# Kernel optimization log

Measured on AMD Instinct MI355X. Metric: run time of the kernel, lower is better.

## Reference

```python
import jax, jax.numpy as jnp
import numpy as np

EMB = 16
N_LEFT = 100000
N_RIGHT = 100000
N_EDGES = 3200000


def setup_inputs() -> dict:
    key = jax.random.key(0)
    ks = jax.random.split(key, 16)
    s = 1.0 / np.sqrt(EMB)
    inp = {
        "left_features": jax.random.normal(ks[0], (N_LEFT, EMB), jnp.float32),
        "edge_indices": jax.random.randint(ks[1], (2, N_EDGES), 0, N_RIGHT, jnp.int64) if jax.config.jax_enable_x64 else jax.random.randint(ks[1], (2, N_EDGES), 0, N_RIGHT, jnp.int32),
        "edge_features": jax.random.normal(ks[2], (N_EDGES, 1), jnp.float32),
        "right_features": jax.random.normal(ks[3], (N_RIGHT, EMB), jnp.float32),
        # feature_module_left: Linear(emb, emb, bias=True)
        "W_left": jax.random.uniform(ks[4], (EMB, EMB), jnp.float32, -s, s),
        "b_left": jax.random.uniform(ks[5], (EMB,), jnp.float32, -s, s),
        # feature_module_edge: Linear(1, emb, bias=False)
        "W_edge": jax.random.uniform(ks[6], (1, EMB), jnp.float32, -1.0, 1.0),
        # feature_module_right: Linear(emb, emb, bias=False)
        "W_right": jax.random.uniform(ks[7], (EMB, EMB), jnp.float32, -s, s),
        # feature_module_final: ReLU -> Linear(emb, emb)
        "W_final": jax.random.uniform(ks[8], (EMB, EMB), jnp.float32, -s, s),
        "b_final": jax.random.uniform(ks[9], (EMB,), jnp.float32, -s, s),
        # post_conv_module: ReLU -> Linear(emb, emb)
        "W_post": jax.random.uniform(ks[10], (EMB, EMB), jnp.float32, -s, s),
        "b_post": jax.random.uniform(ks[11], (EMB,), jnp.float32, -s, s),
        # output_module: Linear(2*emb, emb) -> ReLU -> Linear(emb, emb)
        "W_out1": jax.random.uniform(ks[12], (2 * EMB, EMB), jnp.float32, -1.0 / np.sqrt(2 * EMB), 1.0 / np.sqrt(2 * EMB)),
        "b_out1": jax.random.uniform(ks[13], (EMB,), jnp.float32, -s, s),
        "W_out2": jax.random.uniform(ks[14], (EMB, EMB), jnp.float32, -s, s),
        "b_out2": jax.random.uniform(ks[15], (EMB,), jnp.float32, -s, s),
    }
    return inp


def reference(left_features, edge_indices, edge_features, right_features,
              W_left, b_left, W_edge, W_right, W_final, b_final,
              W_post, b_post, W_out1, b_out1, W_out2, b_out2):
    left_idx = edge_indices[0]
    right_idx = edge_indices[1]
    n_right = right_features.shape[0]

    # per-edge messages: [E, emb]
    msg_left = left_features[left_idx] @ W_left + b_left
    msg_edge = edge_features @ W_edge
    msg_right = right_features[right_idx] @ W_right
    messages = jax.nn.relu(msg_left + msg_edge + msg_right) @ W_final + b_final

    # scatter-add over right nodes
    aggregated = jax.ops.segment_sum(messages, right_idx, num_segments=n_right)

    post = jax.nn.relu(aggregated) @ W_post + b_post
    h = jnp.concatenate([post, right_features], axis=-1)  # [N_right, 2*emb]
    out = jax.nn.relu(h @ W_out1 + b_out1) @ W_out2 + b_out2
    return out
```

## Files before the change

### kernel.cpp

```cpp
#include <hip/hip_runtime.h>

#define EMB 16
#define NPB 196
#define BNODES 256
#define MAXNB 512
#define PCHUNK 6656
#define RPTC 13
#define MAXCHUNKS 512
#define REC_CAP 2048
#define RPT 4
typedef unsigned int u32;
typedef unsigned long long u64;

__global__ void zero_f32(float* __restrict__ p, size_t n) {
    size_t i = (size_t)blockIdx.x * blockDim.x + threadIdx.x;
    size_t stride = (size_t)gridDim.x * blockDim.x;
    for (; i < n; i += stride) p[i] = 0.0f;
}

__global__ void zero_i32(int* __restrict__ p, int n) {
    int i = blockIdx.x * blockDim.x + threadIdx.x;
    if (i < n) p[i] = 0;
}

__device__ __forceinline__ u32 bf16bits_rne(float x) {
    u32 u = __float_as_uint(x);
    return (u + 0x7fffu + ((u >> 16) & 1u)) >> 16;
}

__global__ void linear16_pack_kernel(const float* __restrict__ X, const float* __restrict__ W,
                                     const float* __restrict__ b, u32* __restrict__ Y, int N) {
    int tid = blockIdx.x * blockDim.x + threadIdx.x;
    int row = tid >> 3;
    int h = tid & 7;
    if (row >= N) return;
    float a0 = b ? b[h] : 0.0f;
    float a1 = b ? b[h + 8] : 0.0f;
    const float* xr = X + (size_t)row * EMB;
#pragma unroll
    for (int k = 0; k < EMB; ++k) {
        float xv = xr[k];
        a0 = fmaf(xv, W[k * EMB + h], a0);
        a1 = fmaf(xv, W[k * EMB + h + 8], a1);
    }
    Y[(size_t)row * 8 + h] = (bf16bits_rne(a1) << 16) | bf16bits_rne(a0);
}

__global__ void linear16_kernel(const float* __restrict__ X, const float* __restrict__ W,
                                const float* __restrict__ b, float* __restrict__ Y, int N) {
    int tid = blockIdx.x * blockDim.x + threadIdx.x;
    int row = tid >> 4;
    int j = tid & 15;
    if (row >= N) return;
    float acc = b ? b[j] : 0.0f;
    const float* xr = X + (size_t)row * EMB;
#pragma unroll
    for (int k = 0; k < EMB; ++k) acc = fmaf(xr[k], W[k * EMB + j], acc);
    Y[(size_t)row * EMB + j] = acc;
}

__launch_bounds__(512)
__global__ void chunk_sort_kernel(const int* __restrict__ eidx, const float* __restrict__ ef,
                                  u64* __restrict__ rec, int2* __restrict__ cbM,
                                  int E, int NB, int nchunks) {
    __shared__ u64 srec[PCHUNK];
    __shared__ int hist[MAXNB];
    __shared__ int wsum[8];
    int t = threadIdx.x;
    int lane = t & 63, wid = t >> 6;
    int c = blockIdx.x;
    long long base = (long long)c * PCHUNK;
    int n = (int)(((long long)E - base) < PCHUNK ? ((long long)E - base) : PCHUNK);
    const int* ridx = eidx + E;

    for (int i = t; i < NB; i += 512) hist[i] = 0;
    __syncthreads();
    u64 rcv[RPTC];
    int pk[RPTC];
#pragma unroll
    for (int k = 0; k < RPTC; ++k) {
        int i = t + k * 512;
        rcv[k] = 0; pk[k] = 0;
        if (i < n) {
            int r = ridx[base + i];
            int l = eidx[base + i];
            float f = ef[base + i];
            int bb = r / NPB;
            int rl = r - bb * NPB;
            int rank = atomicAdd(&hist[bb], 1);
            rcv[k] = ((u64)__float_as_uint(f) << 32) | ((u64)(u32)l << 8) | (u32)rl;
            pk[k] = (bb << 13) | rank;
        }
    }
    __syncthreads();
    int v = (t < NB) ? hist[t] : 0;
    int inc = v;
#pragma unroll
    for (int d = 1; d < 64; d <<= 1) {
        int x = __shfl_up(inc, d, 64);
        if (lane >= d) inc += x;
    }
    if (lane == 63) wsum[wid] = inc;
    __syncthreads();
    int off = 0;
#pragma unroll
    for (int w = 0; w < 8; ++w) off += (w < wid) ? wsum[w] : 0;
    int ex = off + inc - v;
    if (t < NB) {
        cbM[(size_t)t * nchunks + c] = make_int2(v, ex);
        hist[t] = ex;
    }
    __syncthreads();
#pragma unroll
    for (int k = 0; k < RPTC; ++k) {
        int i = t + k * 512;
        if (i < n) srec[hist[pk[k] >> 13] + (pk[k] & 8191)] = rcv[k];
    }
    __syncthreads();
    for (int i = t; i < n; i += 512) rec[base + i] = srec[i];
}

__launch_bounds__(512)
__global__ void bucket_gather_kernel(const u64* __restrict__ rec, const int2* __restrict__ cbM,
                                     const u32* __restrict__ Lpk, const u32* __restrict__ Rpk,
                                     const float* __restrict__ We, const float* __restrict__ rf,
                                     const float* __restrict__ Wf, const float* __restrict__ bf,
                                     const float* __restrict__ Wp, const float* __restrict__ bp,
                                     const float* __restrict__ Wo1, const float* __restrict__ bo1,
                                     const float* __restrict__ Wo2, const float* __restrict__ bo2,
                                     float* __restrict__ out,
                                     int n_right, int NB, int nchunks) {
    __shared__ u64 srec[REC_CAP];
    __shared__ u32 addrtab[REC_CAP];
    __shared__ int runsum[MAXCHUNKS + 1];
    __shared__ int rbase[MAXCHUNKS];
    __shared__ int hist[BNODES], base_[BNODES];
    __shared__ int wsum[8];
    __shared__ float sWf[256], sWp[256], sWo1[512], sWo2[256], sb[64];
    int b = blockIdx.x;
    int t = threadIdx.x;
    int lane = t & 63, wid = t >> 6;
    int node0 = b * NPB;

    if (t < 256) { sWf[t] = Wf[t]; sWp[t] = Wp[t]; sWo2[t] = Wo2[t]; }
    sWo1[t] = Wo1[t];
    if (t < 16) { sb[t] = bf[t]; sb[16 + t] = bp[t]; sb[32 + t] = bo1[t]; sb[48 + t] = bo2[t]; }

    int len = 0, cb = 0;
    if (t < nchunks) { int2 v = cbM[(size_t)b * nchunks + t]; len = v.x; cb = v.y; }
    int inc = len;
#pragma unroll
    for (int d = 1; d < 64; d <<= 1) {
        int x = __shfl_up(inc, d, 64);
        if (lane >= d) inc += x;
    }
    if (lane == 63) wsum[wid] = inc;
    __syncthreads();
    int off = 0;
#pragma unroll
    for (int w = 0; w < 8; ++w) off += (w < wid) ? wsum[w] : 0;
    int pexcl = off + inc - len;
    if (t < nchunks) { runsum[t] = pexcl; rbase[t] = t * PCHUNK + cb; }
    if (t == 511) runsum[nchunks] = off + inc;
    __syncthreads();
    int total = runsum[nchunks];

    int n = t >> 1, q = t & 1;
    int node = node0 + n;
    bool nv = (n < NPB) && (node < n_right);

    float we[16];
#pragma unroll
    for (int j = 0; j < 16; ++j) we[j] = We[j];

    float rv[16];
    if (nv) {
        const uint4* rp = (const uint4*)(Rpk + (size_t)node * 8);
        uint4 ra = rp[0], rb = rp[1];
        u32 w0 = ra.x, w1 = ra.y, w2 = ra.z, w3 = ra.w;
        u32 w4 = rb.x, w5 = rb.y, w6 = rb.z, w7 = rb.w;
        rv[0] = __uint_as_float(w0 << 16); rv[8]  = __uint_as_float(w0 & 0xffff0000u);
        rv[1] = __uint_as_float(w1 << 16); rv[9]  = __uint_as_float(w1 & 0xffff0000u);
        rv[2] = __uint_as_float(w2 << 16); rv[10] = __uint_as_float(w2 & 0xffff0000u);
        rv[3] = __uint_as_float(w3 << 16); rv[11] = __uint_as_float(w3 & 0xffff0000u);
        rv[4] = __uint_as_float(w4 << 16); rv[12] = __uint_as_float(w4 & 0xffff0000u);
        rv[5] = __uint_as_float(w5 << 16); rv[13] = __uint_as_float(w5 & 0xffff0000u);
        rv[6] = __uint_as_float(w6 << 16); rv[14] = __uint_as_float(w6 & 0xffff0000u);
        rv[7] = __uint_as_float(w7 << 16); rv[15] = __uint_as_float(w7 & 0xffff0000u);
    } else {
#pragma unroll
        for (int j = 0; j < 16; ++j) rv[j] = 0.0f;
    }

    float acc[16];
#pragma unroll
    for (int j = 0; j < 16; ++j) acc[j] = 0.0f;
    int dsum = 0;

    for (int tile0 = 0; tile0 < total; tile0 += REC_CAP) {
        int m = total - tile0; if (m > REC_CAP) m = REC_CAP;
        u64 rcl[RPT];
        int rnk[RPT];
        if (t < BNODES) hist[t] = 0;
        for (int r = t; r < nchunks; r += 512) {
            int g_lo = runsum[r], g_hi = runsum[r + 1];
            int lo = g_lo > tile0 ? g_lo : tile0;
            int hi = g_hi < tile0 + m ? g_hi : tile0 + m;
            int a = rbase[r] + (lo - g_lo);
            for (int g = lo; g < hi; ++g, ++a) addrtab[g - tile0] = (u32)a;
        }
        __syncthreads();
#pragma unroll
        for (int k = 0; k < RPT; ++k) {
            int i = t + k * 512;
            rcl[k] = (i < m) ? rec[(size_t)addrtab[i]] : 0;
        }
#pragma unroll
        for (int k = 0; k < RPT; ++k) {
            int i = t + k * 512;
            rnk[k] = (i < m) ? atomicAdd(&hist[(int)(rcl[k] & 0xffu)], 1) : 0;
        }
        __syncthreads();
        if (t < 64) {
            int h0 = hist[4 * t], h1 = hist[4 * t + 1], h2 = hist[4 * t + 2], h3 = hist[4 * t + 3];
            int s4 = h0 + h1 + h2 + h3;
            int inc4 = s4;
#pragma unroll
            for (int d = 1; d < 64; d <<= 1) {
                int x = __shfl_up(inc4, d, 64);
                if (t >= d) inc4 += x;
            }
            int ex = inc4 - s4;
            base_[4 * t] = ex;
            base_[4 * t + 1] = ex + h0;
            base_[4 * t + 2] = ex + h0 + h1;
            base_[4 * t + 3] = ex + h0 + h1 + h2;
        }
        __syncthreads();
#pragma unroll
        for (int k = 0; k < RPT; ++k) {
            int i = t + k * 512;
            if (i < m) srec[base_[(int)(rcl[k] & 0xffu)] + rnk[k]] = rcl[k];
        }
        __syncthreads();
        {
            int cc = nv ? hist[n] : 0;
            int b0_ = nv ? base_[n] : 0;
            if (q == 0) dsum += cc;
            for (int k = q; k < cc; k += 2) {
                u64 rc = srec[b0_ + k];
                int l = (int)((rc >> 8) & 0xFFFFFFu);
                float f = __uint_as_float((u32)(rc >> 32));
                const uint4* lp = (const uint4*)(Lpk + (size_t)l * 8);
                uint4 la = lp[0], lb = lp[1];
                u32 w0 = la.x, w1 = la.y, w2 = la.z, w3 = la.w;
                u32 w4 = lb.x, w5 = lb.y, w6 = lb.z, w7 = lb.w;
#define PAIR(h, lw) { \
                float l0 = __uint_as_float(lw << 16); \
                float l1 = __uint_as_float(lw & 0xffff0000u); \
                acc[h]     += fmaxf(fmaf(f, we[h], l0) + rv[h], 0.0f); \
                acc[h + 8] += fmaxf(fmaf(f, we[h + 8], l1) + rv[h + 8], 0.0f); }
                PAIR(0, w0) PAIR(1, w1) PAIR(2, w2) PAIR(3, w3)
                PAIR(4, w4) PAIR(5, w5) PAIR(6, w6) PAIR(7, w7)
#undef PAIR
            }
        }
        __syncthreads();
    }

#pragma unroll
    for (int j = 0; j < 16; ++j) acc[j] += __shfl_xor(acc[j], 1, 64);
    dsum += __shfl_xor(dsum, 1, 64);

    if (nv) {
        float rfx[16];
        const float4* Rf = (const float4*)(rf + (size_t)node * EMB);
#pragma unroll
        for (int k = 0; k < 4; ++k) {
            float4 w = Rf[k];
            rfx[4 * k] = w.x; rfx[4 * k + 1] = w.y; rfx[4 * k + 2] = w.z; rfx[4 * k + 3] = w.w;
        }
        float c = (float)dsum;
        float x[16], y[16], z[16], o[16];
#pragma unroll
        for (int j = 0; j < 16; ++j) {
            float a = c * sb[j];
#pragma unroll
            for (int k = 0; k < 16; ++k) a = fmaf(acc[k], sWf[k * 16 + j], a);
            x[j] = fmaxf(a, 0.0f);
        }
#pragma unroll
        for (int j = 0; j < 16; ++j) {
            float a = sb[16 + j];
#pragma unroll
            for (int k = 0; k < 16; ++k) a = fmaf(x[k], sWp[k * 16 + j], a);
            y[j] = a;
        }
#pragma unroll
        for (int j = 0; j < 16; ++j) {
            float a = sb[32 + j];
#pragma unroll
            for (int k = 0; k < 16; ++k) a = fmaf(y[k], sWo1[k * 16 + j], a);
#pragma unroll
            for (int k = 0; k < 16; ++k) a = fmaf(rfx[k], sWo1[(16 + k) * 16 + j], a);
            z[j] = fmaxf(a, 0.0f);
        }
#pragma unroll
        for (int j = 0; j < 16; ++j) {
            float a = sb[48 + j];
#pragma unroll
            for (int k = 0; k < 16; ++k) a = fmaf(z[k], sWo2[k * 16 + j], a);
            o[j] = a;
        }
        float4* Op = (float4*)(out + (size_t)node * EMB);
        Op[q * 2]     = make_float4(o[q * 8],     o[q * 8 + 1], o[q * 8 + 2], o[q * 8 + 3]);
        Op[q * 2 + 1] = make_float4(o[q * 8 + 4], o[q * 8 + 5], o[q * 8 + 6], o[q * 8 + 7]);
    }
}

__global__ void edge_kernel(const int* __restrict__ eidx, const float* __restrict__ ef,
                            const float* __restrict__ L, const float* __restrict__ R,
                            const float* __restrict__ We, float* __restrict__ S,
                            int* __restrict__ cnt, int E) {
    long long tid = (long long)blockIdx.x * blockDim.x + threadIdx.x;
    int e = (int)(tid >> 4);
    int j = (int)(tid & 15);
    if (e >= E) return;
    int l = eidx[e];
    int r = eidx[E + e];
    float v = L[(size_t)l * EMB + j] + ef[e] * We[j] + R[(size_t)r * EMB + j];
    v = fmaxf(v, 0.0f);
    unsafeAtomicAdd(&S[(size_t)r * EMB + j], v);
    if (j == 0) atomicAdd(&cnt[r], 1);
}

__global__ void final_kernel(const float* __restrict__ S, const int* __restrict__ deg,
                             const float* __restrict__ rf,
                             const float* __restrict__ Wf, const float* __restrict__ bf,
                             const float* __restrict__ Wp, const float* __restrict__ bp,
                             const float* __restrict__ Wo1, const float* __restrict__ bo1,
                             const float* __restrict__ Wo2, const float* __restrict__ bo2,
                             float* __restrict__ out, int N) {
    __shared__ float sWf[256], sWp[256], sWo1[512], sWo2[256];
    __shared__ float sb[64];
    int t = threadIdx.x;
    for (int i = t; i < 256; i += 256) { sWf[i] = Wf[i]; sWp[i] = Wp[i]; sWo2[i] = Wo2[i]; }
    for (int i = t; i < 512; i += 256) sWo1[i] = Wo1[i];
    if (t < 16) { sb[t] = bf[t]; sb[16 + t] = bp[t]; sb[32 + t] = bo1[t]; sb[48 + t] = bo2[t]; }
    __syncthreads();

    int r = blockIdx.x * blockDim.x + t;
    if (r >= N) return;

    float s[16], x[16], y[16], rv[16], z[16], o[16];
    const float4* Sp = (const float4*)(S + (size_t)r * EMB);
    const float4* Rp = (const float4*)(rf + (size_t)r * EMB);
#pragma unroll
    for (int k = 0; k < 4; ++k) {
        float4 v = Sp[k];
        s[4 * k] = v.x; s[4 * k + 1] = v.y; s[4 * k + 2] = v.z; s[4 * k + 3] = v.w;
        float4 w = Rp[k];
        rv[4 * k] = w.x; rv[4 * k + 1] = w.y; rv[4 * k + 2] = w.z; rv[4 * k + 3] = w.w;
    }
    float c = (float)deg[r];

#pragma unroll
    for (int j = 0; j < 16; ++j) {
        float a = c * sb[j];
#pragma unroll
        for (int k = 0; k < 16; ++k) a = fmaf(s[k], sWf[k * 16 + j], a);
        x[j] = fmaxf(a, 0.0f);
    }
#pragma unroll
    for (int j = 0; j < 16; ++j) {
        float a = sb[16 + j];
#pragma unroll
        for (int k = 0; k < 16; ++k) a = fmaf(x[k], sWp[k * 16 + j], a);
        y[j] = a;
    }
#pragma unroll
    for (int j = 0; j < 16; ++j) {
        float a = sb[32 + j];
#pragma unroll
        for (int k = 0; k < 16; ++k) a = fmaf(y[k], sWo1[k * 16 + j], a);
#pragma unroll
        for (int k = 0; k < 16; ++k) a = fmaf(rv[k], sWo1[(16 + k) * 16 + j], a);
        z[j] = fmaxf(a, 0.0f);
    }
#pragma unroll
    for (int j = 0; j < 16; ++j) {
        float a = sb[48 + j];
#pragma unroll
        for (int k = 0; k < 16; ++k) a = fmaf(z[k], sWo2[k * 16 + j], a);
        o[j] = a;
    }
    float4* Op = (float4*)(out + (size_t)r * EMB);
#pragma unroll
    for (int k = 0; k < 4; ++k)
        Op[k] = make_float4(o[4 * k], o[4 * k + 1], o[4 * k + 2], o[4 * k + 3]);
}

extern "C" void kernel_launch(void* const* d_in, const int* in_sizes, int n_in,
                              void* d_out, int out_size, void* d_ws, size_t ws_size,
                              hipStream_t stream) {
    const float* lf     = (const float*)d_in[0];
    const int*   eidx   = (const int*)d_in[1];
    const float* ef     = (const float*)d_in[2];
    const float* rf     = (const float*)d_in[3];
    const float* W_left = (const float*)d_in[4];
    const float* b_left = (const float*)d_in[5];
    const float* W_edge = (const float*)d_in[6];
    const float* W_right= (const float*)d_in[7];
    const float* W_final= (const float*)d_in[8];
    const float* b_final= (const float*)d_in[9];
    const float* W_post = (const float*)d_in[10];
    const float* b_post = (const float*)d_in[11];
    const float* W_out1 = (const float*)d_in[12];
    const float* b_out1 = (const float*)d_in[13];
    const float* W_out2 = (const float*)d_in[14];
    const float* b_out2 = (const float*)d_in[15];

    int n_left  = in_sizes[0] / EMB;
    int E       = in_sizes[2];
    int n_right = in_sizes[3] / EMB;
    float* out = (float*)d_out;

    int NB = (n_right + NPB - 1) / NPB;
    int nchunks = (E + PCHUNK - 1) / PCHUNK;

    size_t need = (size_t)E * 8
                + (size_t)NB * nchunks * 8
                + ((size_t)n_left + n_right) * 32;

    if (ws_size >= need && NB <= MAXNB && nchunks <= MAXCHUNKS) {
        u64*  rec = (u64*)d_ws;
        int2* cbM = (int2*)(rec + (size_t)E);
        u32*  Lpk = (u32*)(cbM + (size_t)NB * nchunks);
        u32*  Rpk = Lpk + (size_t)n_left * 8;

        linear16_pack_kernel<<<(n_left * 8 + 255) / 256, 256, 0, stream>>>(lf, W_left, b_left, Lpk, n_left);
        linear16_pack_kernel<<<(n_right * 8 + 255) / 256, 256, 0, stream>>>(rf, W_right, nullptr, Rpk, n_right);

        chunk_sort_kernel<<<nchunks, 512, 0, stream>>>(eidx, ef, rec, cbM, E, NB, nchunks);

        bucket_gather_kernel<<<NB, 512, 0, stream>>>(rec, cbM, Lpk, Rpk, W_edge, rf,
                                                     W_final, b_final, W_post, b_post,
                                                     W_out1, b_out1, W_out2, b_out2,
                                                     out, n_right, NB, nchunks);
    } else {
        float* L   = (float*)d_ws;
        float* R   = L + (size_t)n_left * EMB;
        float* S   = R + (size_t)n_right * EMB;
        int*   cnt = (int*)(S + (size_t)n_right * EMB);

        zero_f32<<<2048, 256, 0, stream>>>(S, (size_t)n_right * EMB);
        zero_i32<<<(n_right + 255) / 256, 256, 0, stream>>>(cnt, n_right);

        linear16_kernel<<<(n_left * EMB + 255) / 256, 256, 0, stream>>>(lf, W_left, b_left, L, n_left);
        linear16_kernel<<<(n_right * EMB + 255) / 256, 256, 0, stream>>>(rf, W_right, nullptr, R, n_right);

        long long ethreads = (long long)E * EMB;
        edge_kernel<<<(unsigned)((ethreads + 255) / 256), 256, 0, stream>>>(eidx, ef, L, R, W_edge, S, cnt, E);

        final_kernel<<<(n_right + 255) / 256, 256, 0, stream>>>(S, cnt, rf,
            W_final, b_final, W_post, b_post, W_out1, b_out1, W_out2, b_out2, out, n_right);
    }
}
```

Before: 86.65 us.

## Prefetch next record tile during gather and merge the two pack kernels

```diff
diff --git a/kernel.cpp b/kernel.cpp
--- a/kernel.cpp
+++ b/kernel.cpp
@@ -28,22 +28,28 @@
     return (u + 0x7fffu + ((u >> 16) & 1u)) >> 16;
 }
 
-__global__ void linear16_pack_kernel(const float* __restrict__ X, const float* __restrict__ W,
-                                     const float* __restrict__ b, u32* __restrict__ Y, int N) {
+__global__ void pack_both_kernel(const float* __restrict__ lf, const float* __restrict__ rf,
+                                 const float* __restrict__ Wl, const float* __restrict__ bl,
+                                 const float* __restrict__ Wr,
+                                 u32* __restrict__ Lpk, u32* __restrict__ Rpk,
+                                 int n_left, int n_right) {
     int tid = blockIdx.x * blockDim.x + threadIdx.x;
     int row = tid >> 3;
     int h = tid & 7;
-    if (row >= N) return;
-    float a0 = b ? b[h] : 0.0f;
-    float a1 = b ? b[h + 8] : 0.0f;
-    const float* xr = X + (size_t)row * EMB;
+    if (row >= n_left + n_right) return;
+    const float* X; const float* W; const float* bb; u32* Y; int r;
+    if (row < n_left) { X = lf; W = Wl; bb = bl; Y = Lpk; r = row; }
+    else              { X = rf; W = Wr; bb = nullptr; Y = Rpk; r = row - n_left; }
+    float a0 = bb ? bb[h] : 0.0f;
+    float a1 = bb ? bb[h + 8] : 0.0f;
+    const float* xr = X + (size_t)r * EMB;
 #pragma unroll
     for (int k = 0; k < EMB; ++k) {
         float xv = xr[k];
         a0 = fmaf(xv, W[k * EMB + h], a0);
         a1 = fmaf(xv, W[k * EMB + h + 8], a1);
     }
-    Y[(size_t)row * 8 + h] = (bf16bits_rne(a1) << 16) | bf16bits_rne(a0);
+    Y[(size_t)r * 8 + h] = (bf16bits_rne(a1) << 16) | bf16bits_rne(a0);
 }
 
 __global__ void linear16_kernel(const float* __restrict__ X, const float* __restrict__ W,
@@ -134,7 +140,7 @@
     __shared__ u32 addrtab[REC_CAP];
     __shared__ int runsum[MAXCHUNKS + 1];
     __shared__ int rbase[MAXCHUNKS];
-    __shared__ int hist[BNODES], base_[BNODES];
+    __shared__ int hist[BNODES], base_[BNODES + 1];
     __shared__ int wsum[8];
     __shared__ float sWf[256], sWp[256], sWo1[512], sWo2[256], sb[64];
     int b = blockIdx.x;
@@ -162,6 +168,7 @@
     int pexcl = off + inc - len;
     if (t < nchunks) { runsum[t] = pexcl; rbase[t] = t * PCHUNK + cb; }
     if (t == 511) runsum[nchunks] = off + inc;
+    if (t < BNODES) hist[t] = 0;
     __syncthreads();
     int total = runsum[nchunks];
 
@@ -197,24 +204,29 @@
     for (int j = 0; j < 16; ++j) acc[j] = 0.0f;
     int dsum = 0;
 
+    u64 rcl[RPT];
+    {
+        int m0 = total < REC_CAP ? total : REC_CAP;
+        if (m0 > 0) {
+            for (int r = t; r < nchunks; r += 512) {
+                int g_lo = runsum[r], g_hi = runsum[r + 1];
+                int lo = g_lo > 0 ? g_lo : 0;
+                int hi = g_hi < m0 ? g_hi : m0;
+                int a = rbase[r] + (lo - g_lo);
+                for (int g = lo; g < hi; ++g, ++a) addrtab[g] = (u32)a;
+            }
+        }
+        __syncthreads();
+#pragma unroll
+        for (int k = 0; k < RPT; ++k) {
+            int i = t + k * 512;
+            rcl[k] = (i < m0) ? rec[(size_t)addrtab[i]] : 0;
+        }
+    }
+
     for (int tile0 = 0; tile0 < total; tile0 += REC_CAP) {
         int m = total - tile0; if (m > REC_CAP) m = REC_CAP;
-        u64 rcl[RPT];
         int rnk[RPT];
-        if (t < BNODES) hist[t] = 0;
-        for (int r = t; r < nchunks; r += 512) {
-            int g_lo = runsum[r], g_hi = runsum[r + 1];
-            int lo = g_lo > tile0 ? g_lo : tile0;
-            int hi = g_hi < tile0 + m ? g_hi : tile0 + m;
-            int a = rbase[r] + (lo - g_lo);
-            for (int g = lo; g < hi; ++g, ++a) addrtab[g - tile0] = (u32)a;
-        }
-        __syncthreads();
-#pragma unroll
-        for (int k = 0; k < RPT; ++k) {
-            int i = t + k * 512;
-            rcl[k] = (i < m) ? rec[(size_t)addrtab[i]] : 0;
-        }
 #pragma unroll
         for (int k = 0; k < RPT; ++k) {
             int i = t + k * 512;
@@ -235,6 +247,7 @@
             base_[4 * t + 1] = ex + h0;
             base_[4 * t + 2] = ex + h0 + h1;
             base_[4 * t + 3] = ex + h0 + h1 + h2;
+            if (t == 63) base_[BNODES] = inc4;
         }
         __syncthreads();
 #pragma unroll
@@ -242,10 +255,28 @@
             int i = t + k * 512;
             if (i < m) srec[base_[(int)(rcl[k] & 0xffu)] + rnk[k]] = rcl[k];
         }
+        if (t < BNODES) hist[t] = 0;
+        int next0 = tile0 + REC_CAP;
+        int mn = total - next0; if (mn > REC_CAP) mn = REC_CAP;
+        if (mn > 0) {
+            for (int r = t; r < nchunks; r += 512) {
+                int g_lo = runsum[r], g_hi = runsum[r + 1];
+                int lo = g_lo > next0 ? g_lo : next0;
+                int hi = g_hi < next0 + mn ? g_hi : next0 + mn;
+                int a = rbase[r] + (lo - g_lo);
+                for (int g = lo; g < hi; ++g, ++a) addrtab[g - next0] = (u32)a;
+            }
+        }
         __syncthreads();
+        u64 rcln[RPT];
+#pragma unroll
+        for (int k = 0; k < RPT; ++k) {
+            int i = t + k * 512;
+            rcln[k] = (mn > 0 && i < mn) ? rec[(size_t)addrtab[i]] : 0;
+        }
         {
-            int cc = nv ? hist[n] : 0;
             int b0_ = nv ? base_[n] : 0;
+            int cc  = nv ? (base_[n + 1] - b0_) : 0;
             if (q == 0) dsum += cc;
             for (int k = q; k < cc; k += 2) {
                 u64 rc = srec[b0_ + k];
@@ -266,6 +297,8 @@
             }
         }
         __syncthreads();
+#pragma unroll
+        for (int k = 0; k < RPT; ++k) rcl[k] = rcln[k];
     }
 
 #pragma unroll
@@ -438,8 +471,9 @@
         u32*  Lpk = (u32*)(cbM + (size_t)NB * nchunks);
         u32*  Rpk = Lpk + (size_t)n_left * 8;
 
-        linear16_pack_kernel<<<(n_left * 8 + 255) / 256, 256, 0, stream>>>(lf, W_left, b_left, Lpk, n_left);
-        linear16_pack_kernel<<<(n_right * 8 + 255) / 256, 256, 0, stream>>>(rf, W_right, nullptr, Rpk, n_right);
+        int prows = n_left + n_right;
+        pack_both_kernel<<<(prows * 8 + 255) / 256, 256, 0, stream>>>(lf, rf, W_left, b_left, W_right,
+                                                                      Lpk, Rpk, n_left, n_right);
 
         chunk_sort_kernel<<<nchunks, 512, 0, stream>>>(eidx, ef, rec, cbM, E, NB, nchunks);
 
```

New measurement: 79.40 us (median of 2 runs). -8.4%, faster.
